# Optimization experiments

Measured on AMD Instinct MI355X. Metric: run time of the kernel, lower is better.

The kernel has to match this reference:

```python
import jax, jax.numpy as jnp
import numpy as np

N_NODES = 30000
N_EDGES = 480000
B_PAIRS = 4096


def _lin(key, fan_in, fan_out):
    k1, k2 = jax.random.split(key)
    s = 1.0 / np.sqrt(fan_in)
    W = jax.random.uniform(k1, (fan_in, fan_out), minval=-s, maxval=s, dtype=jnp.float32)
    b = jax.random.uniform(k2, (fan_out,), minval=-s, maxval=s, dtype=jnp.float32)
    return W, b


def setup_inputs() -> dict:
    key = jax.random.key(0)
    ks = jax.random.split(key, 20)
    inp = {}
    inp["cid"] = jax.random.normal(ks[0], (N_NODES, 881), dtype=jnp.float32)
    inp["link_edge"] = jax.random.randint(ks[1], (2, N_EDGES), 0, N_NODES, dtype=jnp.int64)
    inp["i1"] = jax.random.randint(ks[2], (B_PAIRS,), 0, N_NODES, dtype=jnp.int64)
    inp["i2"] = jax.random.randint(ks[3], (B_PAIRS,), 0, N_NODES, dtype=jnp.int64)
    inp["soft_thr"] = jnp.array(0.01, jnp.float32)
    inp["bb_fc2_W"], inp["bb_fc2_b"] = _lin(ks[4], 881, 881)
    inp["bb_fc3_W"], inp["bb_fc3_b"] = _lin(ks[5], 881, 256)
    inp["gcn1_W"], inp["gcn1_b"] = _lin(ks[6], 256, 256)
    inp["gcn2_W"], inp["gcn2_b"] = _lin(ks[7], 256, 256)
    inp["gcn3_W"], inp["gcn3_b"] = _lin(ks[8], 256, 256)
    inp["gcn4_W"], inp["gcn4_b"] = _lin(ks[9], 256, 128)
    inp["gcn5_W"], inp["gcn5_b"] = _lin(ks[10], 128, 128)
    inp["fc1_W"], inp["fc1_b"] = _lin(ks[11], 256, 1024)
    inp["fc2_W"], inp["fc2_b"] = _lin(ks[12], 1024, 256)
    inp["fc3_W"], inp["fc3_b"] = _lin(ks[13], 256, 64)
    inp["out_W"], inp["out_b"] = _lin(ks[14], 64, 2)
    return inp


def _forward(cid, link_edge, i1, i2, soft_thr,
             bb_fc2_W, bb_fc2_b, bb_fc3_W, bb_fc3_b,
             gcn1_W, gcn1_b, gcn2_W, gcn2_b, gcn3_W, gcn3_b,
             gcn4_W, gcn4_b, gcn5_W, gcn5_b,
             fc1_W, fc1_b, fc2_W, fc2_b, fc3_W, fc3_b, out_W, out_b):
    N = cid.shape[0]
    # --- BasicBlock1 (eval mode, dropout off everywhere) ---
    x = jax.nn.relu(cid @ bb_fc2_W + bb_fc2_b)
    x = jnp.sign(x) * jax.nn.relu(jnp.abs(x) - soft_thr)  # soft threshold
    x = jax.nn.relu(x @ bb_fc3_W + bb_fc3_b)              # [N, 256]

    # --- GCN normalization (PyG GCNConv: add self-loops, sym norm) ---
    loop = jnp.arange(N, dtype=link_edge.dtype)
    src = jnp.concatenate([link_edge[0], loop])
    dst = jnp.concatenate([link_edge[1], loop])
    deg = jax.ops.segment_sum(jnp.ones_like(dst, dtype=jnp.float32), dst, num_segments=N)
    dinv = jnp.where(deg > 0, jax.lax.rsqrt(deg), 0.0)
    enorm = (dinv[src] * dinv[dst])[:, None]  # [E+N, 1]

    def gcn(h, W, b):
        h = h @ W                                            # [N, F_out]
        msg = h[src] * enorm                                 # gather + scale
        return jax.ops.segment_sum(msg, dst, num_segments=N) + b

    h = jax.nn.elu(gcn(x, gcn1_W, gcn1_b))
    h = jax.nn.elu(gcn(h, gcn2_W, gcn2_b))
    h = jax.nn.elu(gcn(h, gcn3_W, gcn3_b))
    h = jax.nn.elu(gcn(h, gcn4_W, gcn4_b))
    h = jax.nn.elu(gcn(h, gcn5_W, gcn5_b))                   # [N, 128]

    # --- pair readout ---
    xc = jnp.concatenate([h[i1], h[i2]], axis=1)             # [B, 256]
    norm = jnp.maximum(jnp.linalg.norm(xc, axis=1, keepdims=True), 1e-12)
    xc = xc / norm                                           # F.normalize(p=2, dim=1)
    xc = jax.nn.relu(xc @ fc1_W + fc1_b)
    xc = jax.nn.relu(xc @ fc2_W + fc2_b)
    xc = jax.nn.relu(xc @ fc3_W + fc3_b)
    return xc @ out_W + out_b                                # [B, 2]


def reference(cid, link_edge, i1, i2, soft_thr,
              bb_fc2_W, bb_fc2_b, bb_fc3_W, bb_fc3_b,
              gcn1_W, gcn1_b, gcn2_W, gcn2_b, gcn3_W, gcn3_b,
              gcn4_W, gcn4_b, gcn5_W, gcn5_b,
              fc1_W, fc1_b, fc2_W, fc2_b, fc3_W, fc3_b, out_W, out_b):
    return _forward(cid, link_edge, i1, i2, soft_thr,
                    bb_fc2_W, bb_fc2_b, bb_fc3_W, bb_fc3_b,
                    gcn1_W, gcn1_b, gcn2_W, gcn2_b, gcn3_W, gcn3_b,
                    gcn4_W, gcn4_b, gcn5_W, gcn5_b,
                    fc1_W, fc1_b, fc2_W, fc2_b, fc3_W, fc3_b, out_W, out_b)
```

## Files before the change

### kernel.cpp

```cpp
#include <hip/hip_runtime.h>
#include <hip/hip_bf16.h>
#include <math.h>


#define NNODES 30000
#define NEDGES 480000
#define NPAIRS 4096

typedef __attribute__((ext_vector_type(8))) short short8;
typedef __attribute__((ext_vector_type(4))) short short4v;
typedef __attribute__((ext_vector_type(2))) short short2v;
typedef __attribute__((ext_vector_type(4))) float f32x4;
typedef __attribute__((ext_vector_type(2))) float f32x2;
typedef unsigned short u16;

__device__ __forceinline__ u16 f2bf(float x) {
    union { float f; unsigned u; } v; v.f = x;
    unsigned u = v.u;
    return (u16)((u + 0x7FFFu + ((u >> 16) & 1u)) >> 16);
}
__device__ __forceinline__ float bf2f(u16 h) {
    union { float f; unsigned u; } v; v.u = ((unsigned)h) << 16;
    return v.f;
}

__device__ __forceinline__ void gll16(const u16* g, u16* l) {
    __builtin_amdgcn_global_load_lds(
        (const __attribute__((address_space(1))) unsigned int*)g,
        (__attribute__((address_space(3))) unsigned int*)l, 16, 0, 0);
}


__global__ void k_count(const int* __restrict__ dst, unsigned* __restrict__ cnt, int E) {
    int e = blockIdx.x * blockDim.x + threadIdx.x;
    if (e < E) atomicAdd(&cnt[dst[e]], 1u);
}

__global__ void k_dinv(const unsigned* __restrict__ cnt, float* __restrict__ dinv, int N) {
    int n = blockIdx.x * blockDim.x + threadIdx.x;
    if (n < N) {
        float deg = (float)(cnt[n] + 1u);
        dinv[n] = 1.0f / sqrtf(deg);
    }
}

__global__ void k_scan(const unsigned* __restrict__ cnt, unsigned* __restrict__ rowptr, int N) {
    __shared__ unsigned buf[1024];
    __shared__ unsigned carry_s;
    const int tid = threadIdx.x;
    if (tid == 0) { carry_s = 0; rowptr[0] = 0; }
    __syncthreads();
    for (int base = 0; base < N; base += 1024) {
        int i = base + tid;
        unsigned v = (i < N) ? cnt[i] : 0u;
        buf[tid] = v;
        __syncthreads();
        for (int off = 1; off < 1024; off <<= 1) {
            unsigned t = (tid >= off) ? buf[tid - off] : 0u;
            __syncthreads();
            buf[tid] += t;
            __syncthreads();
        }
        unsigned c = carry_s;
        if (i < N) rowptr[i + 1] = c + buf[tid];
        __syncthreads();
        if (tid == 1023) carry_s = c + buf[1023];
        __syncthreads();
    }
}

__global__ void k_fill(const int* __restrict__ src, const int* __restrict__ dst,
                       const unsigned* __restrict__ rowptr, unsigned* __restrict__ cursor,
                       int* __restrict__ colsrc, int E) {
    int e = blockIdx.x * blockDim.x + threadIdx.x;
    if (e < E) {
        int d = dst[e];
        unsigned p = atomicAdd(&cursor[d], 1u);
        colsrc[rowptr[d] + p] = src[e];
    }
}


__global__ void k_wconv(const float* __restrict__ W, u16* __restrict__ Th,
                        u16* __restrict__ Tl, int K, int N, int Kp, int Np) {
    int idx = blockIdx.x * blockDim.x + threadIdx.x;
    if (idx >= Np * Kp) return;
    int n = idx / Kp, k = idx - n * Kp;
    float v = (n < N && k < K) ? W[(size_t)k * N + n] : 0.f;
    u16 h = f2bf(v);
    Th[idx] = h;
    Tl[idx] = f2bf(v - bf2f(h));
}


template <int ASRC, int EPI, int OUTM>
__global__ __launch_bounds__(256) void k_mgemm(
    const float* __restrict__ Af, int ldAf, int Ktrue,
    const u16* __restrict__ Ahi, const u16* __restrict__ Alo, int ldA,
    const u16* __restrict__ Bhi, const u16* __restrict__ Blo, int ldB,
    const float* __restrict__ bias, const float* __restrict__ thrp,
    const float* __restrict__ rowscale,
    float* __restrict__ Cf, u16* __restrict__ Chi, u16* __restrict__ Clo,
    int ldC, int M, int Ntrue, int K, int gy) {
    __shared__ alignas(16) u16 Ah[128 * 32];
    __shared__ alignas(16) u16 Al[128 * 32];
    __shared__ alignas(16) u16 Bh[128 * 32];
    __shared__ alignas(16) u16 Bl[128 * 32];
    const int t = threadIdx.x;
    const int lane = t & 63, w = t >> 6;
    const int wr = w >> 1, wc = w & 1;
    const int r16 = lane & 15, kg = lane >> 4;
    const int nwg = gridDim.x;
    const int q = nwg >> 3, r = nwg & 7;
    const int xcd = blockIdx.x & 7, pos = blockIdx.x >> 3;
    const int wg = (xcd < r ? xcd * (q + 1) : r * (q + 1) + (xcd - r) * q) + pos;
    const int bx = wg / gy, by = wg - bx * gy;
    const int bm = bx * 128, bn = by * 128;
    const int srow = (w << 5) + (lane >> 2);
    const int k8 = (lane & 3) << 3;
    const int lb = w << 11;
    f32x4 acc[4][4] = {};

    for (int k0 = 0; k0 < K; k0 += 32) {
        if (ASRC == 0) {
            const int arow = t >> 1, kq = (t & 1) << 4;
            int gm = bm + arow; if (gm >= M) gm = M - 1;
            const size_t base = (size_t)gm * ldAf;
#pragma unroll
            for (int jj = 0; jj < 2; ++jj) {
                short8 hv, lv;
#pragma unroll
                for (int j = 0; j < 8; ++j) {
                    const int k = k0 + kq + jj * 8 + j;
                    float v = (k < Ktrue) ? Af[base + k] : 0.f;
                    u16 hh = f2bf(v);
                    hv[j] = (short)hh;
                    lv[j] = (short)f2bf(v - bf2f(hh));
                }
                *(short8*)&Ah[arow * 32 + kq + jj * 8] = hv;
                *(short8*)&Al[arow * 32 + kq + jj * 8] = lv;
            }
        } else {
            gll16(Ahi + (size_t)(bm + srow) * ldA + k0 + k8, (u16*)((char*)Ah + lb));
            gll16(Ahi + (size_t)(bm + srow + 16) * ldA + k0 + k8, (u16*)((char*)Ah + lb + 1024));
            gll16(Alo + (size_t)(bm + srow) * ldA + k0 + k8, (u16*)((char*)Al + lb));
            gll16(Alo + (size_t)(bm + srow + 16) * ldA + k0 + k8, (u16*)((char*)Al + lb + 1024));
        }
        gll16(Bhi + (size_t)(bn + srow) * ldB + k0 + k8, (u16*)((char*)Bh + lb));
        gll16(Bhi + (size_t)(bn + srow + 16) * ldB + k0 + k8, (u16*)((char*)Bh + lb + 1024));
        gll16(Blo + (size_t)(bn + srow) * ldB + k0 + k8, (u16*)((char*)Bl + lb));
        gll16(Blo + (size_t)(bn + srow + 16) * ldB + k0 + k8, (u16*)((char*)Bl + lb + 1024));
        __syncthreads();
        short8 fah[4], fal[4];
#pragma unroll
        for (int mi = 0; mi < 4; ++mi) {
            const int off = (wr * 64 + mi * 16 + r16) * 32 + kg * 8;
            fah[mi] = *(const short8*)&Ah[off];
            fal[mi] = *(const short8*)&Al[off];
        }
#pragma unroll
        for (int ni = 0; ni < 4; ++ni) {
            const int off = (wc * 64 + ni * 16 + r16) * 32 + kg * 8;
            const short8 fbh = *(const short8*)&Bh[off];
            const short8 fbl = *(const short8*)&Bl[off];
#pragma unroll
            for (int mi = 0; mi < 4; ++mi) {
                acc[mi][ni] = __builtin_amdgcn_mfma_f32_16x16x32_bf16(fah[mi], fbh, acc[mi][ni], 0, 0, 0);
                acc[mi][ni] = __builtin_amdgcn_mfma_f32_16x16x32_bf16(fal[mi], fbh, acc[mi][ni], 0, 0, 0);
                acc[mi][ni] = __builtin_amdgcn_mfma_f32_16x16x32_bf16(fah[mi], fbl, acc[mi][ni], 0, 0, 0);
            }
        }
        __syncthreads();
    }

    const float thr = (EPI == 2) ? *thrp : 0.f;
#pragma unroll
    for (int mi = 0; mi < 4; ++mi) {
#pragma unroll
        for (int i = 0; i < 4; ++i) {
            const int m = bm + wr * 64 + mi * 16 + kg * 4 + i;
            if (m >= M) continue;
            const float rs = (OUTM == 2) ? rowscale[m] : 1.f;
#pragma unroll
            for (int ni = 0; ni < 4; ++ni) {
                const int n = bn + wc * 64 + ni * 16 + r16;
                float z = acc[mi][ni][i];
                if (EPI >= 1) {
                    z += (n < Ntrue) ? bias[n] : 0.f;
                    z = (EPI == 1) ? fmaxf(z, 0.f) : fmaxf(z - thr, 0.f);
                }
                if (OUTM == 0) {
                    if (n < Ntrue) Cf[(size_t)m * ldC + n] = z;
                } else if (OUTM == 2) {
                    if (n < Ntrue) Cf[(size_t)m * ldC + n] = z * rs;
                } else {
                    if (n < ldC) {
                        if (n >= Ntrue) z = 0.f;
                        u16 h = f2bf(z);
                        size_t o = (size_t)m * ldC + n;
                        Chi[o] = h;
                        Clo[o] = f2bf(z - bf2f(h));
                    }
                }
            }
        }
    }
}


template <int FV, int WB>
__global__ __launch_bounds__(256) void k_agg(
    const float* __restrict__ hWs, const float* __restrict__ dinv,
    const unsigned* __restrict__ rowptr, const int* __restrict__ colsrc,
    const float* __restrict__ bias, float* __restrict__ outf,
    u16* __restrict__ oh, u16* __restrict__ ol, int N) {
    const int wave = threadIdx.x >> 6;
    const int lane = threadIdx.x & 63;
    const int n = blockIdx.x * 4 + wave;
    if (n >= N) return;
    const int F = FV * 64;
    const int fb = lane * FV;
    float acc[FV];
    if (FV == 4) {
        const f32x4 v = *(const f32x4*)(hWs + (size_t)n * F + fb);
#pragma unroll
        for (int j = 0; j < FV; ++j) acc[j] = v[j];
    } else {
        const f32x2 v = *(const f32x2*)(hWs + (size_t)n * F + fb);
#pragma unroll
        for (int j = 0; j < FV; ++j) acc[j] = v[j];
    }
    unsigned idx = rowptr[n];
    const unsigned end = rowptr[n + 1];
    for (; idx + 2 <= end; idx += 2) {
        int s0 = colsrc[idx], s1 = colsrc[idx + 1];
        if (FV == 4) {
            const f32x4 v0 = *(const f32x4*)(hWs + (size_t)s0 * F + fb);
            const f32x4 v1 = *(const f32x4*)(hWs + (size_t)s1 * F + fb);
#pragma unroll
            for (int j = 0; j < FV; ++j) acc[j] += v0[j] + v1[j];
        } else {
            const f32x2 v0 = *(const f32x2*)(hWs + (size_t)s0 * F + fb);
            const f32x2 v1 = *(const f32x2*)(hWs + (size_t)s1 * F + fb);
#pragma unroll
            for (int j = 0; j < FV; ++j) acc[j] += v0[j] + v1[j];
        }
    }
    if (idx < end) {
        int s0 = colsrc[idx];
        if (FV == 4) {
            const f32x4 v0 = *(const f32x4*)(hWs + (size_t)s0 * F + fb);
#pragma unroll
            for (int j = 0; j < FV; ++j) acc[j] += v0[j];
        } else {
            const f32x2 v0 = *(const f32x2*)(hWs + (size_t)s0 * F + fb);
#pragma unroll
            for (int j = 0; j < FV; ++j) acc[j] += v0[j];
        }
    }
    const float dn = dinv[n];
    float z[FV];
#pragma unroll
    for (int j = 0; j < FV; ++j) {
        float zz = dn * acc[j] + bias[fb + j];
        z[j] = (zz > 0.f) ? zz : expm1f(zz);
    }
    if (WB) {
        if (FV == 4) {
            short4v hv, lv;
#pragma unroll
            for (int j = 0; j < 4; ++j) {
                u16 h = f2bf(z[j]);
                hv[j] = (short)h;
                lv[j] = (short)f2bf(z[j] - bf2f(h));
            }
            *(short4v*)(oh + (size_t)n * F + fb) = hv;
            *(short4v*)(ol + (size_t)n * F + fb) = lv;
        } else {
            short2v hv, lv;
#pragma unroll
            for (int j = 0; j < 2; ++j) {
                u16 h = f2bf(z[j]);
                hv[j] = (short)h;
                lv[j] = (short)f2bf(z[j] - bf2f(h));
            }
            *(short2v*)(oh + (size_t)n * F + fb) = hv;
            *(short2v*)(ol + (size_t)n * F + fb) = lv;
        }
    } else {
        if (FV == 4) {
            f32x4 v;
#pragma unroll
            for (int j = 0; j < 4; ++j) v[j] = z[j];
            *(f32x4*)(outf + (size_t)n * F + fb) = v;
        } else {
            f32x2 v;
#pragma unroll
            for (int j = 0; j < 2; ++j) v[j] = z[j];
            *(f32x2*)(outf + (size_t)n * F + fb) = v;
        }
    }
}


__global__ __launch_bounds__(256) void k_pairs(
    const float* __restrict__ h, const int* __restrict__ i1, const int* __restrict__ i2,
    u16* __restrict__ xh, u16* __restrict__ xl, int B) {
    const int wave = threadIdx.x >> 6;
    const int lane = threadIdx.x & 63;
    const int p = blockIdx.x * 4 + wave;
    if (p >= B) return;
    const int a = i1[p], b = i2[p];
    float v0 = h[(size_t)a * 128 + lane];
    float v1 = h[(size_t)a * 128 + 64 + lane];
    float v2 = h[(size_t)b * 128 + lane];
    float v3 = h[(size_t)b * 128 + 64 + lane];
    float ss = v0 * v0 + v1 * v1 + v2 * v2 + v3 * v3;
#pragma unroll
    for (int o = 32; o > 0; o >>= 1) ss += __shfl_xor(ss, o, 64);
    float scale = 1.0f / fmaxf(sqrtf(ss), 1e-12f);
    size_t o = (size_t)p * 256;
    float vv[4] = {v0 * scale, v1 * scale, v2 * scale, v3 * scale};
#pragma unroll
    for (int j = 0; j < 4; ++j) {
        u16 hh = f2bf(vv[j]);
        xh[o + j * 64 + lane] = hh;
        xl[o + j * 64 + lane] = f2bf(vv[j] - bf2f(hh));
    }
}

__global__ __launch_bounds__(256) void k_out(
    const float* __restrict__ x, const float* __restrict__ W, const float* __restrict__ b,
    float* __restrict__ out, int B) {
    const int wave = threadIdx.x >> 6;
    const int lane = threadIdx.x & 63;
    const int p = blockIdx.x * 4 + wave;
    if (p >= B) return;
    float v = x[(size_t)p * 64 + lane];
    float s0 = v * W[lane * 2 + 0];
    float s1 = v * W[lane * 2 + 1];
#pragma unroll
    for (int o = 32; o > 0; o >>= 1) {
        s0 += __shfl_xor(s0, o, 64);
        s1 += __shfl_xor(s1, o, 64);
    }
    if (lane == 0) {
        out[p * 2 + 0] = s0 + b[0];
        out[p * 2 + 1] = s1 + b[1];
    }
}


extern "C" void kernel_launch(void* const* d_in, const int* in_sizes, int n_in,
                              void* d_out, int out_size, void* d_ws, size_t ws_size,
                              hipStream_t stream) {
    const float* cid = (const float*)d_in[0];
    const int* le   = (const int*)d_in[1];
    const int* i1   = (const int*)d_in[2];
    const int* i2   = (const int*)d_in[3];
    const float* thr = (const float*)d_in[4];
    const float* W2 = (const float*)d_in[5];  const float* b2 = (const float*)d_in[6];
    const float* W3 = (const float*)d_in[7];  const float* b3 = (const float*)d_in[8];
    const float* gW[5] = {(const float*)d_in[9],  (const float*)d_in[11], (const float*)d_in[13],
                          (const float*)d_in[15], (const float*)d_in[17]};
    const float* gB[5] = {(const float*)d_in[10], (const float*)d_in[12], (const float*)d_in[14],
                          (const float*)d_in[16], (const float*)d_in[18]};
    const float* fc1W = (const float*)d_in[19]; const float* fc1b = (const float*)d_in[20];
    const float* fc2W = (const float*)d_in[21]; const float* fc2b = (const float*)d_in[22];
    const float* fc3W = (const float*)d_in[23]; const float* fc3b = (const float*)d_in[24];
    const float* oW   = (const float*)d_in[25]; const float* ob   = (const float*)d_in[26];

    const int N = NNODES, E = NEDGES, B = NPAIRS;
    char* ws = (char*)d_ws;

    unsigned* cnt    = (unsigned*)(ws + 0);
    unsigned* cursor = (unsigned*)(ws + 120064);
    unsigned* rowptr = (unsigned*)(ws + 240128);
    int*      colsrc = (int*)     (ws + 360192);
    float*    dinv   = (float*)   (ws + 2280192);

    u16* W2th = (u16*)(ws + 2400256);  u16* W2tl = (u16*)(ws + 4005888);
    u16* W3th = (u16*)(ws + 5611520);  u16* W3tl = (u16*)(ws + 6070272);
    u16* g1h  = (u16*)(ws + 6529024);  u16* g1l  = (u16*)(ws + 6660096);
    u16* g2h  = (u16*)(ws + 6791168);  u16* g2l  = (u16*)(ws + 6922240);
    u16* g3h  = (u16*)(ws + 7053312);  u16* g3l  = (u16*)(ws + 7184384);
    u16* g4h  = (u16*)(ws + 7315456);  u16* g4l  = (u16*)(ws + 7380992);
    u16* g5h  = (u16*)(ws + 7446528);  u16* g5l  = (u16*)(ws + 7479296);
    u16* f1h  = (u16*)(ws + 7512064);  u16* f1l  = (u16*)(ws + 8036352);
    u16* f2h  = (u16*)(ws + 8560640);  u16* f2l  = (u16*)(ws + 9084928);
    u16* f3h  = (u16*)(ws + 9609216);  u16* f3l  = (u16*)(ws + 9674752);

    u16* x2h = (u16*)(ws + 9740288);
    u16* x2l = (u16*)(ws + 25141248);
    const size_t X1 = 40542208;
    u16* x1h = (u16*)(ws + X1);
    u16* x1l = (u16*)(ws + X1 + 53903360);
    float* hWs  = (float*)(ws + X1);
    u16*   hAh  = (u16*)  (ws + X1 + 30801920);
    u16*   hAl  = (u16*)  (ws + X1 + 46202880);
    float* hfin = (float*)(ws + X1 + 61603840);
    u16*   xch  = (u16*)  (ws + X1 + 76963840);
    u16*   xcl  = (u16*)  (ws + X1 + 79060992);
    u16*   t1h  = (u16*)  (ws + X1 + 81158144);
    u16*   t1l  = (u16*)  (ws + X1 + 89546752);
    u16*   t2h  = (u16*)  (ws + X1 + 97935360);
    u16*   t2l  = (u16*)  (ws + X1 + 100032512);
    float* t3   = (float*)(ws + X1 + 102129664);

    hipMemsetAsync(cnt, 0, N * sizeof(unsigned), stream);
    hipMemsetAsync(cursor, 0, N * sizeof(unsigned), stream);
    k_count<<<(E + 255) / 256, 256, 0, stream>>>(le + E, cnt, E);
    k_dinv<<<(N + 255) / 256, 256, 0, stream>>>(cnt, dinv, N);
    k_scan<<<1, 1024, 0, stream>>>(cnt, rowptr, N);
    k_fill<<<(E + 255) / 256, 256, 0, stream>>>(le, le + E, rowptr, cursor, colsrc, E);

    k_wconv<<<3136, 256, 0, stream>>>(W2, W2th, W2tl, 881, 881, 896, 896);
    k_wconv<<<896, 256, 0, stream>>>(W3, W3th, W3tl, 881, 256, 896, 256);
    k_wconv<<<256, 256, 0, stream>>>(gW[0], g1h, g1l, 256, 256, 256, 256);
    k_wconv<<<256, 256, 0, stream>>>(gW[1], g2h, g2l, 256, 256, 256, 256);
    k_wconv<<<256, 256, 0, stream>>>(gW[2], g3h, g3l, 256, 256, 256, 256);
    k_wconv<<<128, 256, 0, stream>>>(gW[3], g4h, g4l, 256, 128, 256, 128);
    k_wconv<<<64, 256, 0, stream>>>(gW[4], g5h, g5l, 128, 128, 128, 128);
    k_wconv<<<1024, 256, 0, stream>>>(fc1W, f1h, f1l, 256, 1024, 256, 1024);
    k_wconv<<<1024, 256, 0, stream>>>(fc2W, f2h, f2l, 1024, 256, 1024, 256);
    k_wconv<<<128, 256, 0, stream>>>(fc3W, f3h, f3l, 256, 64, 256, 128);

    const int MB = (N + 127) / 128;

    k_mgemm<0, 2, 1><<<MB * 7, 256, 0, stream>>>(
        cid, 881, 881, nullptr, nullptr, 0, W2th, W2tl, 896, b2, thr, nullptr,
        nullptr, x1h, x1l, 896, N, 881, 896, 7);
    k_mgemm<1, 1, 1><<<MB * 2, 256, 0, stream>>>(
        nullptr, 0, 0, x1h, x1l, 896, W3th, W3tl, 896, b3, nullptr, nullptr,
        nullptr, x2h, x2l, 256, N, 256, 896, 2);

    const u16* wh[5] = {g1h, g2h, g3h, g4h, g5h};
    const u16* wl[5] = {g1l, g2l, g3l, g4l, g5l};
    const int fin[5]  = {256, 256, 256, 256, 128};
    const int fout[5] = {256, 256, 256, 128, 128};
    u16* curh = x2h;  u16* curl = x2l;
    for (int l = 0; l < 5; ++l) {
        const int gy = fout[l] / 128;
        k_mgemm<1, 0, 2><<<MB * gy, 256, 0, stream>>>(
            nullptr, 0, 0, curh, curl, fin[l], wh[l], wl[l], fin[l], nullptr, nullptr, dinv,
            hWs, nullptr, nullptr, fout[l], N, fout[l], fin[l], gy);
        if (l == 4) {
            k_agg<2, 0><<<(N + 3) / 4, 256, 0, stream>>>(hWs, dinv, rowptr, colsrc, gB[l],
                                                         hfin, nullptr, nullptr, N);
        } else if (fout[l] == 256) {
            u16* oh = (l & 1) ? x2h : hAh;
            u16* ol = (l & 1) ? x2l : hAl;
            k_agg<4, 1><<<(N + 3) / 4, 256, 0, stream>>>(hWs, dinv, rowptr, colsrc, gB[l],
                                                         nullptr, oh, ol, N);
            curh = oh; curl = ol;
        } else {
            k_agg<2, 1><<<(N + 3) / 4, 256, 0, stream>>>(hWs, dinv, rowptr, colsrc, gB[l],
                                                         nullptr, x2h, x2l, N);
            curh = x2h; curl = x2l;
        }
    }

    k_pairs<<<(B + 3) / 4, 256, 0, stream>>>(hfin, i1, i2, xch, xcl, B);
    k_mgemm<1, 1, 1><<<32 * 8, 256, 0, stream>>>(
        nullptr, 0, 0, xch, xcl, 256, f1h, f1l, 256, fc1b, nullptr, nullptr,
        nullptr, t1h, t1l, 1024, B, 1024, 256, 8);
    k_mgemm<1, 1, 1><<<32 * 2, 256, 0, stream>>>(
        nullptr, 0, 0, t1h, t1l, 1024, f2h, f2l, 1024, fc2b, nullptr, nullptr,
        nullptr, t2h, t2l, 256, B, 256, 1024, 2);
    k_mgemm<1, 1, 0><<<32 * 1, 256, 0, stream>>>(
        nullptr, 0, 0, t2h, t2l, 256, f3h, f3l, 256, fc3b, nullptr, nullptr,
        t3, nullptr, nullptr, 64, B, 64, 256, 1);
    k_out<<<(B + 3) / 4, 256, 0, stream>>>(t3, oW, ob, (float*)d_out, B);
}
```

Baseline: 1.360 ms.

## Pre-split cid to bf16 pairs, prefetch A registers, unroll GCN aggregation by four

When the workspace is large enough, a new kernel converts cid once into padded bf16 hi/lo arrays, so the first GEMM can use the async global-to-LDS path instead of converting fp32 inside every column block. The workspace layout is reworked to make room for this. The fp32-A GEMM path now prefetches the next K-slice of A into registers while the current slice is computed, and B loads are issued before the A conversion. The aggregation kernel gathers four neighbours per iteration instead of two, to raise memory-level parallelism. The trade-offs are an extra full pass writing a 107MB intermediate, and a fast path that depends on a workspace-size threshold.

```diff
diff --git a/kernel.cpp b/kernel.cpp
--- a/kernel.cpp
+++ b/kernel.cpp
@@ -90,6 +90,17 @@
     u16 h = f2bf(v);
     Th[idx] = h;
     Tl[idx] = f2bf(v - bf2f(h));
+}
+
+__global__ void k_aconv(const float* __restrict__ A, u16* __restrict__ Hh,
+                        u16* __restrict__ Hl) {
+    int idx = blockIdx.x * blockDim.x + threadIdx.x;
+    if (idx >= NNODES * 896) return;
+    int row = idx / 896, col = idx - row * 896;
+    float v = (col < 881) ? A[(size_t)row * 881 + col] : 0.f;
+    u16 h = f2bf(v);
+    Hh[idx] = h;
+    Hl[idx] = f2bf(v - bf2f(h));
 }
 
 
@@ -121,36 +132,52 @@
     const int lb = w << 11;
     f32x4 acc[4][4] = {};
 
+    const int arow = t >> 1, kq = (t & 1) << 4;
+    int gmA = bm + arow; if (gmA >= M) gmA = M - 1;
+    const float* aBase = (ASRC == 0) ? (Af + (size_t)gmA * ldAf) : nullptr;
+    float aR[16];
+
+    auto LOADA = [&](int k0) {
+#pragma unroll
+        for (int j = 0; j < 16; ++j) aR[j] = aBase[k0 + kq + j];
+    };
+    auto WRITEA = [&](int k0) {
+        short8 hv0, lv0, hv1, lv1;
+#pragma unroll
+        for (int j = 0; j < 8; ++j) {
+            float v = (k0 + kq + j < Ktrue) ? aR[j] : 0.f;
+            u16 hh = f2bf(v);
+            hv0[j] = (short)hh;
+            lv0[j] = (short)f2bf(v - bf2f(hh));
+        }
+#pragma unroll
+        for (int j = 0; j < 8; ++j) {
+            float v = (k0 + kq + 8 + j < Ktrue) ? aR[8 + j] : 0.f;
+            u16 hh = f2bf(v);
+            hv1[j] = (short)hh;
+            lv1[j] = (short)f2bf(v - bf2f(hh));
+        }
+        const int wa = arow * 32 + kq;
+        *(short8*)&Ah[wa] = hv0;  *(short8*)&Ah[wa + 8] = hv1;
+        *(short8*)&Al[wa] = lv0;  *(short8*)&Al[wa + 8] = lv1;
+    };
+
+    if (ASRC == 0) LOADA(0);
     for (int k0 = 0; k0 < K; k0 += 32) {
+        gll16(Bhi + (size_t)(bn + srow) * ldB + k0 + k8, (u16*)((char*)Bh + lb));
+        gll16(Bhi + (size_t)(bn + srow + 16) * ldB + k0 + k8, (u16*)((char*)Bh + lb + 1024));
+        gll16(Blo + (size_t)(bn + srow) * ldB + k0 + k8, (u16*)((char*)Bl + lb));
+        gll16(Blo + (size_t)(bn + srow + 16) * ldB + k0 + k8, (u16*)((char*)Bl + lb + 1024));
         if (ASRC == 0) {
-            const int arow = t >> 1, kq = (t & 1) << 4;
-            int gm = bm + arow; if (gm >= M) gm = M - 1;
-            const size_t base = (size_t)gm * ldAf;
-#pragma unroll
-            for (int jj = 0; jj < 2; ++jj) {
-                short8 hv, lv;
-#pragma unroll
-                for (int j = 0; j < 8; ++j) {
-                    const int k = k0 + kq + jj * 8 + j;
-                    float v = (k < Ktrue) ? Af[base + k] : 0.f;
-                    u16 hh = f2bf(v);
-                    hv[j] = (short)hh;
-                    lv[j] = (short)f2bf(v - bf2f(hh));
-                }
-                *(short8*)&Ah[arow * 32 + kq + jj * 8] = hv;
-                *(short8*)&Al[arow * 32 + kq + jj * 8] = lv;
-            }
+            WRITEA(k0);
         } else {
             gll16(Ahi + (size_t)(bm + srow) * ldA + k0 + k8, (u16*)((char*)Ah + lb));
             gll16(Ahi + (size_t)(bm + srow + 16) * ldA + k0 + k8, (u16*)((char*)Ah + lb + 1024));
             gll16(Alo + (size_t)(bm + srow) * ldA + k0 + k8, (u16*)((char*)Al + lb));
             gll16(Alo + (size_t)(bm + srow + 16) * ldA + k0 + k8, (u16*)((char*)Al + lb + 1024));
         }
-        gll16(Bhi + (size_t)(bn + srow) * ldB + k0 + k8, (u16*)((char*)Bh + lb));
-        gll16(Bhi + (size_t)(bn + srow + 16) * ldB + k0 + k8, (u16*)((char*)Bh + lb + 1024));
-        gll16(Blo + (size_t)(bn + srow) * ldB + k0 + k8, (u16*)((char*)Bl + lb));
-        gll16(Blo + (size_t)(bn + srow + 16) * ldB + k0 + k8, (u16*)((char*)Bl + lb + 1024));
         __syncthreads();
+        if (ASRC == 0 && k0 + 32 < K) LOADA(k0 + 32);
         short8 fah[4], fal[4];
 #pragma unroll
         for (int mi = 0; mi < 4; ++mi) {
@@ -220,40 +247,47 @@
     if (n >= N) return;
     const int F = FV * 64;
     const int fb = lane * FV;
+    const float* __restrict__ hbase = hWs + fb;
     float acc[FV];
-    if (FV == 4) {
-        const f32x4 v = *(const f32x4*)(hWs + (size_t)n * F + fb);
-#pragma unroll
-        for (int j = 0; j < FV; ++j) acc[j] = v[j];
-    } else {
-        const f32x2 v = *(const f32x2*)(hWs + (size_t)n * F + fb);
-#pragma unroll
-        for (int j = 0; j < FV; ++j) acc[j] = v[j];
+    {
+        if (FV == 4) {
+            const f32x4 v = *(const f32x4*)(hbase + (size_t)n * F);
+#pragma unroll
+            for (int j = 0; j < FV; ++j) acc[j] = v[j];
+        } else {
+            const f32x2 v = *(const f32x2*)(hbase + (size_t)n * F);
+#pragma unroll
+            for (int j = 0; j < FV; ++j) acc[j] = v[j];
+        }
     }
     unsigned idx = rowptr[n];
     const unsigned end = rowptr[n + 1];
-    for (; idx + 2 <= end; idx += 2) {
-        int s0 = colsrc[idx], s1 = colsrc[idx + 1];
+    for (; idx + 4 <= end; idx += 4) {
+        int s0 = colsrc[idx], s1 = colsrc[idx + 1], s2 = colsrc[idx + 2], s3 = colsrc[idx + 3];
         if (FV == 4) {
-            const f32x4 v0 = *(const f32x4*)(hWs + (size_t)s0 * F + fb);
-            const f32x4 v1 = *(const f32x4*)(hWs + (size_t)s1 * F + fb);
-#pragma unroll
-            for (int j = 0; j < FV; ++j) acc[j] += v0[j] + v1[j];
-        } else {
-            const f32x2 v0 = *(const f32x2*)(hWs + (size_t)s0 * F + fb);
-            const f32x2 v1 = *(const f32x2*)(hWs + (size_t)s1 * F + fb);
-#pragma unroll
-            for (int j = 0; j < FV; ++j) acc[j] += v0[j] + v1[j];
-        }
-    }
-    if (idx < end) {
+            const f32x4 v0 = *(const f32x4*)(hbase + (size_t)s0 * F);
+            const f32x4 v1 = *(const f32x4*)(hbase + (size_t)s1 * F);
+            const f32x4 v2 = *(const f32x4*)(hbase + (size_t)s2 * F);
+            const f32x4 v3 = *(const f32x4*)(hbase + (size_t)s3 * F);
+#pragma unroll
+            for (int j = 0; j < FV; ++j) acc[j] += (v0[j] + v1[j]) + (v2[j] + v3[j]);
+        } else {
+            const f32x2 v0 = *(const f32x2*)(hbase + (size_t)s0 * F);
+            const f32x2 v1 = *(const f32x2*)(hbase + (size_t)s1 * F);
+            const f32x2 v2 = *(const f32x2*)(hbase + (size_t)s2 * F);
+            const f32x2 v3 = *(const f32x2*)(hbase + (size_t)s3 * F);
+#pragma unroll
+            for (int j = 0; j < FV; ++j) acc[j] += (v0[j] + v1[j]) + (v2[j] + v3[j]);
+        }
+    }
+    for (; idx < end; ++idx) {
         int s0 = colsrc[idx];
         if (FV == 4) {
-            const f32x4 v0 = *(const f32x4*)(hWs + (size_t)s0 * F + fb);
+            const f32x4 v0 = *(const f32x4*)(hbase + (size_t)s0 * F);
 #pragma unroll
             for (int j = 0; j < FV; ++j) acc[j] += v0[j];
         } else {
-            const f32x2 v0 = *(const f32x2*)(hWs + (size_t)s0 * F + fb);
+            const f32x2 v0 = *(const f32x2*)(hbase + (size_t)s0 * F);
 #pragma unroll
             for (int j = 0; j < FV; ++j) acc[j] += v0[j];
         }
@@ -372,13 +406,13 @@
 
     const int N = NNODES, E = NEDGES, B = NPAIRS;
     char* ws = (char*)d_ws;
+    const bool big = ws_size >= 230000000ull;
 
     unsigned* cnt    = (unsigned*)(ws + 0);
     unsigned* cursor = (unsigned*)(ws + 120064);
     unsigned* rowptr = (unsigned*)(ws + 240128);
     int*      colsrc = (int*)     (ws + 360192);
     float*    dinv   = (float*)   (ws + 2280192);
-
     u16* W2th = (u16*)(ws + 2400256);  u16* W2tl = (u16*)(ws + 4005888);
     u16* W3th = (u16*)(ws + 5611520);  u16* W3tl = (u16*)(ws + 6070272);
     u16* g1h  = (u16*)(ws + 6529024);  u16* g1l  = (u16*)(ws + 6660096);
@@ -390,22 +424,47 @@
     u16* f2h  = (u16*)(ws + 8560640);  u16* f2l  = (u16*)(ws + 9084928);
     u16* f3h  = (u16*)(ws + 9609216);  u16* f3l  = (u16*)(ws + 9674752);
 
-    u16* x2h = (u16*)(ws + 9740288);
-    u16* x2l = (u16*)(ws + 25141248);
-    const size_t X1 = 40542208;
-    u16* x1h = (u16*)(ws + X1);
-    u16* x1l = (u16*)(ws + X1 + 53903360);
-    float* hWs  = (float*)(ws + X1);
-    u16*   hAh  = (u16*)  (ws + X1 + 30801920);
-    u16*   hAl  = (u16*)  (ws + X1 + 46202880);
-    float* hfin = (float*)(ws + X1 + 61603840);
-    u16*   xch  = (u16*)  (ws + X1 + 76963840);
-    u16*   xcl  = (u16*)  (ws + X1 + 79060992);
-    u16*   t1h  = (u16*)  (ws + X1 + 81158144);
-    u16*   t1l  = (u16*)  (ws + X1 + 89546752);
-    u16*   t2h  = (u16*)  (ws + X1 + 97935360);
-    u16*   t2l  = (u16*)  (ws + X1 + 100032512);
-    float* t3   = (float*)(ws + X1 + 102129664);
+    u16 *cidh = nullptr, *cidl = nullptr;
+    u16 *x1h, *x1l, *x2h, *x2l, *hAh, *hAl, *xch, *xcl, *t1h, *t1l, *t2h, *t2l;
+    float *hWs, *hfin, *t3;
+    if (big) {
+        const size_t CB = 9740288;
+        const size_t XB = CB + 2ull * 53903360;
+        cidh = (u16*)(ws + CB);
+        cidl = (u16*)(ws + CB + 53903360);
+        x1h  = (u16*)(ws + XB);
+        x1l  = (u16*)(ws + XB + 53903360);
+        x2h  = (u16*)(ws + CB);
+        x2l  = (u16*)(ws + CB + 15400960);
+        hWs  = (float*)(ws + CB + 30801920);
+        hfin = (float*)(ws + CB + 61603840);
+        xch  = (u16*)(ws + CB + 76963840);
+        xcl  = (u16*)(ws + CB + 79060992);
+        t1h  = (u16*)(ws + CB + 81158144);
+        t1l  = (u16*)(ws + CB + 89546752);
+        t2h  = (u16*)(ws + CB + 97935360);
+        t2l  = (u16*)(ws + CB + 100032512);
+        t3   = (float*)(ws + CB + 102129664);
+        hAh  = (u16*)(ws + XB);
+        hAl  = (u16*)(ws + XB + 15400960);
+    } else {
+        const size_t X1 = 40542208;
+        x2h = (u16*)(ws + 9740288);
+        x2l = (u16*)(ws + 25141248);
+        x1h = (u16*)(ws + X1);
+        x1l = (u16*)(ws + X1 + 53903360);
+        hWs  = (float*)(ws + X1);
+        hAh  = (u16*)  (ws + X1 + 30801920);
+        hAl  = (u16*)  (ws + X1 + 46202880);
+        hfin = (float*)(ws + X1 + 61603840);
+        xch  = (u16*)  (ws + X1 + 76963840);
+        xcl  = (u16*)  (ws + X1 + 79060992);
+        t1h  = (u16*)  (ws + X1 + 81158144);
+        t1l  = (u16*)  (ws + X1 + 89546752);
+        t2h  = (u16*)  (ws + X1 + 97935360);
+        t2l  = (u16*)  (ws + X1 + 100032512);
+        t3   = (float*)(ws + X1 + 102129664);
+    }
 
     hipMemsetAsync(cnt, 0, N * sizeof(unsigned), stream);
     hipMemsetAsync(cursor, 0, N * sizeof(unsigned), stream);
@@ -427,9 +486,16 @@
 
     const int MB = (N + 127) / 128;
 
-    k_mgemm<0, 2, 1><<<MB * 7, 256, 0, stream>>>(
-        cid, 881, 881, nullptr, nullptr, 0, W2th, W2tl, 896, b2, thr, nullptr,
-        nullptr, x1h, x1l, 896, N, 881, 896, 7);
+    if (big) {
+        k_aconv<<<(NNODES * 896 + 255) / 256, 256, 0, stream>>>(cid, cidh, cidl);
+        k_mgemm<1, 2, 1><<<MB * 7, 256, 0, stream>>>(
+            nullptr, 0, 0, cidh, cidl, 896, W2th, W2tl, 896, b2, thr, nullptr,
+            nullptr, x1h, x1l, 896, N, 881, 896, 7);
+    } else {
+        k_mgemm<0, 2, 1><<<MB * 7, 256, 0, stream>>>(
+            cid, 881, 881, nullptr, nullptr, 0, W2th, W2tl, 896, b2, thr, nullptr,
+            nullptr, x1h, x1l, 896, N, 881, 896, 7);
+    }
     k_mgemm<1, 1, 1><<<MB * 2, 256, 0, stream>>>(
         nullptr, 0, 0, x1h, x1l, 896, W3th, W3tl, 896, b3, nullptr, nullptr,
         nullptr, x2h, x2l, 256, N, 256, 896, 2);
```

Result: faster. 1.174 ms (-13.7%).
